# Performance work log

Hardware: AMD Instinct MI355X
Metric: run time of the kernel (lower is better)

The kernel has to match this reference:

```python
import jax, jax.numpy as jnp
import numpy as np
from jax import lax

NUM_MASK_PARAMS = 67  # 66 weights (64 feat + 2 coord channels) + 1 bias
NUM_GEN_PARAMS = 134


def _coord_maps(h, w, dtype):
    yy = jnp.broadcast_to(jnp.linspace(-1.0, 1.0, h, dtype=dtype)[:, None], (h, w))
    xx = jnp.broadcast_to(jnp.linspace(-1.0, 1.0, w, dtype=dtype)[None, :], (h, w))
    return xx, yy


def _dynamic_head(x_cat, p):
    # x_cat: [66, H, W]; p: [num_ins, 67] -> [num_ins, H, W]
    w = p[:, :NUM_MASK_PARAMS - 1]
    b = p[:, NUM_MASK_PARAMS - 1]
    return jnp.einsum('ic,chw->ihw', w, x_cat) + b[:, None, None]


def setup_inputs() -> dict:
    key = jax.random.key(0)
    ks = jax.random.split(key, 10)
    C, HM, WM, HH, WH, MB, HID = 256, 272, 480, 136, 240, 64, 64
    rn = lambda k, s, sc=1.0: jax.random.normal(k, s, dtype=jnp.float32) * sc
    return {
        'out0': rn(ks[0], (1, C, HM, WM)),
        'out1': rn(ks[1], (1, C, HH, WH)),
        'hm_w': rn(ks[2], (1, C), 0.05),
        'hm_b': jnp.zeros((1,), jnp.float32),
        'params_w': rn(ks[3], (NUM_GEN_PARAMS, C), 0.05),
        'params_b': rn(ks[4], (NUM_GEN_PARAMS,), 0.05),
        'mb_w': rn(ks[5], (MB, C, 3, 3), 0.05),
        'mb_b': jnp.zeros((MB,), jnp.float32),
        'mlp_w1': rn(ks[6], (HM, HID), 0.05),
        'mlp_b1': jnp.zeros((HID,), jnp.float32),
        'mlp_w2': rn(ks[7], (HID, 2), 0.05),
        'mlp_b2': jnp.zeros((2,), jnp.float32),
        'num_ins': 4,
    }


def reference(out0, out1, hm_w, hm_b, params_w, params_b, mb_w, mb_b,
              mlp_w1, mlp_b1, mlp_w2, mlp_b2, num_ins):
    h_mask, w_mask = out0.shape[2], out0.shape[3]
    h_hm, w_hm = out1.shape[2], out1.shape[3]

    # ctnet head: 1x1 convs on the stride-16 feature
    hm = jnp.einsum('kc,bchw->bkhw', hm_w, out1) + hm_b[None, :, None, None]
    params = jnp.einsum('kc,bchw->bkhw', params_w, out1) + params_b[None, :, None, None]
    hm = jnp.clip(jax.nn.sigmoid(hm), 1e-4, 1.0 - 1e-4)  # [1,1,h_hm,w_hm]
    # [1,134,h,w] -> [h*w, 134]
    params_flat = jnp.transpose(params[0], (1, 2, 0)).reshape(-1, NUM_GEN_PARAMS)

    # 3x3 maxpool NMS (stride 1, pad 1), keep only local peaks
    hmax = lax.reduce_window(hm, -jnp.inf, lax.max, (1, 1, 3, 3), (1, 1, 1, 1),
                             [(0, 0), (0, 0), (1, 1), (1, 1)])
    keep = (hmax == hm).astype(hm.dtype)
    heat_nms = (hm * keep).reshape(-1)

    scores, inds = lax.top_k(heat_nms, num_ins)

    # mask branch: 3x3 conv + relu on the stride-8 feature
    mask_branch = lax.conv_general_dilated(out0, mb_w, (1, 1), 'SAME',
                                           dimension_numbers=('NCHW', 'OIHW', 'NCHW'))
    mask_branch = jax.nn.relu(mask_branch + mb_b[None, :, None, None])  # [1,64,H,W]

    xx, yy = _coord_maps(h_mask, w_mask, mask_branch.dtype)
    x_cat = jnp.concatenate([mask_branch[0], xx[None], yy[None]], axis=0)  # [66,H,W]

    gen_params = params_flat[inds]  # [num_ins, 134]
    masks0 = _dynamic_head(x_cat, gen_params[:, :NUM_MASK_PARAMS])   # [num_ins,H,W]
    regs0 = _dynamic_head(x_cat, gen_params[:, NUM_MASK_PARAMS:])    # [num_ins,H,W]

    # row-wise vertical-range MLP over h_mask
    feat_range = jnp.transpose(masks0, (0, 2, 1))  # [num_ins, w_mask, h_mask]
    h1 = jax.nn.relu(feat_range @ mlp_w1 + mlp_b1)
    feat_range = h1 @ mlp_w2 + mlp_b2  # [num_ins, w_mask, 2]

    return scores, inds, regs0, masks0, feat_range
```

## Files before the change

### kernel.cpp

```cpp
#include <hip/hip_runtime.h>
#include <math.h>
#include <limits.h>

#define C_IN 256
#define HM_H 136
#define HM_W 240
#define HM_N (HM_H * HM_W)
#define MB   64
#define MH   272
#define MW   480
#define MN   (MH * MW)
#define NP   134
#define NI   4
#define HID  64

#define REG_OFF   8
#define MASK_OFF  (8 + NI * MN)
#define FEAT_OFF  (8 + 2 * NI * MN)

#define WS_HM   0
#define WS_CV   HM_N
#define WS_CI   (HM_N + 512)
#define WS_GP   (2 * HM_N)
#define WS_INDS (2 * HM_N + NI * NP)
#define WS_WT_F 65824

typedef float  f32x4  __attribute__((ext_vector_type(4)));
typedef short  bf16x8 __attribute__((ext_vector_type(8)));

__device__ __forceinline__ unsigned short f2bf(float f) {
  unsigned int u = __float_as_uint(f);
  u += 0x7FFFu + ((u >> 16) & 1u);
  return (unsigned short)(u >> 16);
}
__device__ __forceinline__ float b2f(unsigned short h) {
  return __uint_as_float(((unsigned int)h) << 16);
}

__global__ void k_wprep(const float* __restrict__ mb_w, unsigned short* __restrict__ wt) {
  int idx = blockIdx.x * 256 + threadIdx.x;
  int j    = idx & 7;
  int lane = (idx >> 3) & 63;
  int nt   = (idx >> 9) & 3;
  int gt   = idx >> 11;
  int t    = gt % 9;
  int g    = gt / 9;
  int n = nt * 16 + (lane & 15);
  int c = g * 32 + (lane >> 4) * 8 + j;
  wt[idx] = f2bf(mb_w[(n * C_IN + c) * 9 + t]);
}

__global__ void k_hm(const float* __restrict__ out1, const float* __restrict__ hm_w,
                     const float* __restrict__ hm_b, float* __restrict__ ws_hm) {
  __shared__ float part[4][64];
  int b = blockIdx.x, t = threadIdx.x;
  int cg = t >> 6, pl = t & 63;
  int p = b * 64 + pl;
  float s = 0.f;
  #pragma unroll 16
  for (int c = 0; c < 64; ++c)
    s += hm_w[cg * 64 + c] * out1[(cg * 64 + c) * HM_N + p];
  part[cg][pl] = s;
  __syncthreads();
  if (t < 64) {
    float tot = part[0][t] + part[1][t] + part[2][t] + part[3][t] + hm_b[0];
    float sig = 1.f / (1.f + expf(-tot));
    sig = fminf(fmaxf(sig, 1e-4f), 1.f - 1e-4f);
    ws_hm[b * 64 + t] = sig;
  }
}

__device__ __forceinline__ bool better(float av, int ai, float bv, int bi) {
  return (av > bv) || (av == bv && ai < bi);
}

template<int NTHR>
__device__ void top4_tree(float* sv, int* si, int t) {
  for (int s = NTHR / 2; s >= 1; s >>= 1) {
    if (t < s) {
      float a[4], b[4]; int ai[4], bj[4];
      #pragma unroll
      for (int k = 0; k < 4; ++k) {
        a[k] = sv[t * 4 + k];        ai[k] = si[t * 4 + k];
        b[k] = sv[(t + s) * 4 + k];  bj[k] = si[(t + s) * 4 + k];
      }
      float ov[4]; int oi[4];
      int i = 0, j = 0;
      #pragma unroll
      for (int k = 0; k < 4; ++k) {
        if (better(a[i], ai[i], b[j], bj[j])) { ov[k] = a[i]; oi[k] = ai[i]; ++i; }
        else                                   { ov[k] = b[j]; oi[k] = bj[j]; ++j; }
      }
      #pragma unroll
      for (int k = 0; k < 4; ++k) { sv[t * 4 + k] = ov[k]; si[t * 4 + k] = oi[k]; }
    }
    __syncthreads();
  }
}

__global__ void k_nms_top(const float* __restrict__ ws_hm, float* __restrict__ candv,
                          int* __restrict__ candi) {
  __shared__ float sv[256 * 4];
  __shared__ int   si[256 * 4];
  int b = blockIdx.x, t = threadIdx.x;
  float v = -1.f; int idx = INT_MAX;
  if (t < 255) {
    int p = b * 255 + t;
    int y = p / HM_W, x = p - y * HM_W;
    float c = ws_hm[p], m = c;
    #pragma unroll
    for (int dy = -1; dy <= 1; ++dy)
      #pragma unroll
      for (int dx = -1; dx <= 1; ++dx) {
        int yy = y + dy, xx = x + dx;
        if (yy >= 0 && yy < HM_H && xx >= 0 && xx < HM_W)
          m = fmaxf(m, ws_hm[yy * HM_W + xx]);
      }
    v = (c == m) ? c : 0.f;
    idx = p;
  }
  sv[t * 4] = v; si[t * 4] = idx;
  #pragma unroll
  for (int k = 1; k < 4; ++k) { sv[t * 4 + k] = -1.f; si[t * 4 + k] = INT_MAX; }
  __syncthreads();
  top4_tree<256>(sv, si, t);
  if (t == 0) {
    #pragma unroll
    for (int k = 0; k < 4; ++k) { candv[b * 4 + k] = sv[k]; candi[b * 4 + k] = si[k]; }
  }
}

__global__ void k_topk_final(const float* __restrict__ candv, const int* __restrict__ candi,
                             int* __restrict__ ws_inds, float* __restrict__ d_out) {
  __shared__ float sv[128 * 4];
  __shared__ int   si[128 * 4];
  int t = threadIdx.x;
  #pragma unroll
  for (int k = 0; k < 4; ++k) { sv[t * 4 + k] = candv[t * 4 + k]; si[t * 4 + k] = candi[t * 4 + k]; }
  __syncthreads();
  top4_tree<128>(sv, si, t);
  if (t == 0) {
    #pragma unroll
    for (int k = 0; k < 4; ++k) {
      d_out[k]     = sv[k];
      d_out[4 + k] = (float)si[k];
      ws_inds[k]   = si[k];
    }
  }
}

__global__ void k_gen(const float* __restrict__ out1, const float* __restrict__ params_w,
                      const float* __restrict__ params_b, const int* __restrict__ ws_inds,
                      float* __restrict__ ws_gp) {
  __shared__ float col[C_IN];
  int i = blockIdx.x;
  int p = ws_inds[i];
  col[threadIdx.x] = out1[threadIdx.x * HM_N + p];
  __syncthreads();
  int j = threadIdx.x;
  if (j < NP) {
    float s = params_b[j];
    #pragma unroll 8
    for (int c = 0; c < C_IN; ++c) s += params_w[j * C_IN + c] * col[c];
    ws_gp[i * NP + j] = s;
  }
}

#define CS 40
#define RP 36
#define BUFU 14400

__global__ __launch_bounds__(256, 2) void k_conv_mfma(
    const float* __restrict__ out0, const unsigned short* __restrict__ wt,
    const float* __restrict__ mb_b, const float* __restrict__ ws_gp,
    float* __restrict__ d_out) {
  __shared__ unsigned short smem[2 * BUFU];

  int tid  = threadIdx.x;
  int lane = tid & 63;
  int w    = tid >> 6;
  int n15  = lane & 15;
  int kq   = lane >> 4;
  int gx0 = blockIdx.x * 32, gy0 = blockIdx.y * 8;

  int goff[25], lofs[25];
  unsigned int mld = 0, mst0 = 0, mst1 = 0;
  #pragma unroll
  for (int i = 0; i < 25; ++i) {
    int u = tid + 256 * i;
    int c   = u / 200;
    int rem = u - c * 200;
    int row = rem / 20;
    int q   = rem - row * 20;
    int iy  = gy0 + row - 1;
    int ixe = gx0 + 2 * q - 2;
    bool vld = (iy >= 0) && (iy < MH) && (ixe >= 0) && (ixe < MW);
    goff[i] = vld ? (c * MN + iy * MW + ixe) : 0;
    if (vld) mld |= (1u << i);
    int x0 = 2 * q - 1;
    lofs[i] = (row * RP + x0) * CS + c;
    if (x0 >= 0 && x0 < RP)     mst0 |= (1u << i);
    if (x0 + 1 < RP)            mst1 |= (1u << i);
  }

  int rrow[4], xbas[4];
  #pragma unroll
  for (int i = 0; i < 4; ++i) {
    int mt = w * 4 + i;
    rrow[i] = mt >> 1;
    xbas[i] = (mt & 1) * 16 + n15;
  }

  {
    float2 d[25];
    #pragma unroll
    for (int i = 0; i < 25; ++i) d[i] = *(const float2*)(out0 + goff[i]);
    #pragma unroll
    for (int i = 0; i < 25; ++i) {
      bool vl = (mld >> i) & 1;
      float a = vl ? d[i].x : 0.f, bb = vl ? d[i].y : 0.f;
      if ((mst0 >> i) & 1) smem[lofs[i]]      = f2bf(a);
      if ((mst1 >> i) & 1) smem[lofs[i] + CS] = f2bf(bb);
    }
  }
  __syncthreads();

  f32x4 acc[4][4];
  #pragma unroll
  for (int i = 0; i < 4; ++i)
    #pragma unroll
    for (int nt = 0; nt < 4; ++nt)
      acc[i][nt] = (f32x4){0.f, 0.f, 0.f, 0.f};

  #pragma unroll 1
  for (int g = 0; g < 8; ++g) {
    const unsigned short* cur = smem + (g & 1) * BUFU;
    unsigned short*       nxt = smem + ((g + 1) & 1) * BUFU;
    const float*          src = out0 + (g + 1) * (32 * MN);
    float2 d[25];

    if (g < 7) {
      #pragma unroll
      for (int i = 0; i < 13; ++i) d[i] = *(const float2*)(src + goff[i]);
    }
    #pragma unroll
    for (int t = 0; t < 4; ++t) {
      int ty = t / 3, tx = t - ty * 3;
      const unsigned short* wb = wt + (g * 9 + t) * 2048 + lane * 8;
      bf16x8 bfrag[4], afrag[4];
      #pragma unroll
      for (int nt = 0; nt < 4; ++nt) bfrag[nt] = *(const bf16x8*)(wb + nt * 512);
      #pragma unroll
      for (int i = 0; i < 4; ++i)
        afrag[i] = *(const bf16x8*)&cur[((rrow[i] + ty) * RP + xbas[i] + tx) * CS + kq * 8];
      #pragma unroll
      for (int i = 0; i < 4; ++i)
        #pragma unroll
        for (int nt = 0; nt < 4; ++nt)
          acc[i][nt] = __builtin_amdgcn_mfma_f32_16x16x32_bf16(afrag[i], bfrag[nt], acc[i][nt], 0, 0, 0);
    }
    if (g < 7) {
      #pragma unroll
      for (int i = 0; i < 13; ++i) {
        bool vl = (mld >> i) & 1;
        float a = vl ? d[i].x : 0.f, bb = vl ? d[i].y : 0.f;
        if ((mst0 >> i) & 1) nxt[lofs[i]]      = f2bf(a);
        if ((mst1 >> i) & 1) nxt[lofs[i] + CS] = f2bf(bb);
      }
      #pragma unroll
      for (int i = 13; i < 25; ++i) d[i] = *(const float2*)(src + goff[i]);
    }
    #pragma unroll
    for (int t = 4; t < 9; ++t) {
      int ty = t / 3, tx = t - ty * 3;
      const unsigned short* wb = wt + (g * 9 + t) * 2048 + lane * 8;
      bf16x8 bfrag[4], afrag[4];
      #pragma unroll
      for (int nt = 0; nt < 4; ++nt) bfrag[nt] = *(const bf16x8*)(wb + nt * 512);
      #pragma unroll
      for (int i = 0; i < 4; ++i)
        afrag[i] = *(const bf16x8*)&cur[((rrow[i] + ty) * RP + xbas[i] + tx) * CS + kq * 8];
      #pragma unroll
      for (int i = 0; i < 4; ++i)
        #pragma unroll
        for (int nt = 0; nt < 4; ++nt)
          acc[i][nt] = __builtin_amdgcn_mfma_f32_16x16x32_bf16(afrag[i], bfrag[nt], acc[i][nt], 0, 0, 0);
    }
    if (g < 7) {
      #pragma unroll
      for (int i = 13; i < 25; ++i) {
        bool vl = (mld >> i) & 1;
        float a = vl ? d[i].x : 0.f, bb = vl ? d[i].y : 0.f;
        if ((mst0 >> i) & 1) nxt[lofs[i]]      = f2bf(a);
        if ((mst1 >> i) & 1) nxt[lofs[i] + CS] = f2bf(bb);
      }
    }
    __syncthreads();
  }

  #define ES 66
  float bias[4];
  #pragma unroll
  for (int nt = 0; nt < 4; ++nt) bias[nt] = mb_b[nt * 16 + n15];
  #pragma unroll
  for (int i = 0; i < 4; ++i) {
    int mt = w * 4 + i;
    int pbase = (mt >> 1) * 32 + (mt & 1) * 16;
    #pragma unroll
    for (int nt = 0; nt < 4; ++nt)
      #pragma unroll
      for (int reg = 0; reg < 4; ++reg) {
        float vv = fmaxf(acc[i][nt][reg] + bias[nt], 0.f);
        smem[(pbase + kq * 4 + reg) * ES + nt * 16 + n15] = f2bf(vv);
      }
  }
  __syncthreads();

  int r = tid >> 5, xcol = tid & 31;
  int gy = gy0 + r, gx = gx0 + xcol;
  float xc = -1.f + (2.f / 479.f) * (float)gx;
  float yc = -1.f + (2.f / 271.f) * (float)gy;
  float mres[4] = {0.f, 0.f, 0.f, 0.f};
  float rres[4] = {0.f, 0.f, 0.f, 0.f};
  #pragma unroll 8
  for (int o = 0; o < MB; ++o) {
    float v = b2f(smem[tid * ES + o]);
    #pragma unroll
    for (int i = 0; i < 4; ++i) {
      mres[i] += ws_gp[i * NP + o] * v;
      rres[i] += ws_gp[i * NP + 67 + o] * v;
    }
  }
  int pix = gy * MW + gx;
  #pragma unroll
  for (int i = 0; i < 4; ++i) {
    const float* g = ws_gp + i * NP;
    d_out[MASK_OFF + i * MN + pix] = mres[i] + g[66]  + g[64]  * xc + g[65]  * yc;
    d_out[REG_OFF  + i * MN + pix] = rres[i] + g[133] + g[131] * xc + g[132] * yc;
  }
}

__global__ void k_mlp(const float* __restrict__ masks0, const float* __restrict__ w1,
                      const float* __restrict__ b1, const float* __restrict__ w2,
                      const float* __restrict__ b2, float* __restrict__ d_out) {
  int blk = blockIdx.x;
  int i = blk / MW;
  int w = blk - i * MW;
  int k = threadIdx.x;
  const float* mcol = masks0 + i * MN + w;
  float s = b1[k];
  for (int h = 0; h < MH; ++h) s += mcol[h * MW] * w1[h * HID + k];
  s = fmaxf(s, 0.f);
  float o0 = s * w2[k * 2 + 0];
  float o1 = s * w2[k * 2 + 1];
  #pragma unroll
  for (int off = 32; off >= 1; off >>= 1) {
    o0 += __shfl_down(o0, off);
    o1 += __shfl_down(o1, off);
  }
  if (k == 0) {
    d_out[FEAT_OFF + blk * 2 + 0] = o0 + b2[0];
    d_out[FEAT_OFF + blk * 2 + 1] = o1 + b2[1];
  }
}

extern "C" void kernel_launch(void* const* d_in, const int* in_sizes, int n_in,
                              void* d_out, int out_size, void* d_ws, size_t ws_size,
                              hipStream_t stream) {
  const float* out0     = (const float*)d_in[0];
  const float* out1     = (const float*)d_in[1];
  const float* hm_w     = (const float*)d_in[2];
  const float* hm_b     = (const float*)d_in[3];
  const float* params_w = (const float*)d_in[4];
  const float* params_b = (const float*)d_in[5];
  const float* mb_w     = (const float*)d_in[6];
  const float* mb_b     = (const float*)d_in[7];
  const float* mlp_w1   = (const float*)d_in[8];
  const float* mlp_b1   = (const float*)d_in[9];
  const float* mlp_w2   = (const float*)d_in[10];
  const float* mlp_b2   = (const float*)d_in[11];

  float* ws      = (float*)d_ws;
  float* ws_hm   = ws + WS_HM;
  float* candv   = ws + WS_CV;
  int*   candi   = (int*)(ws + WS_CI);
  float* ws_gp   = ws + WS_GP;
  int*   ws_inds = (int*)(ws + WS_INDS);
  unsigned short* ws_wt = (unsigned short*)(ws + WS_WT_F);
  float* out     = (float*)d_out;

  k_wprep<<<576, 256, 0, stream>>>(mb_w, ws_wt);
  k_hm  <<<510, 256, 0, stream>>>(out1, hm_w, hm_b, ws_hm);
  k_nms_top<<<128, 256, 0, stream>>>(ws_hm, candv, candi);
  k_topk_final<<<1, 128, 0, stream>>>(candv, candi, ws_inds, out);
  k_gen <<<NI, 256, 0, stream>>>(out1, params_w, params_b, ws_inds, ws_gp);
  dim3 gconv(MW / 32, MH / 8);
  k_conv_mfma<<<gconv, 256, 0, stream>>>(out0, ws_wt, mb_b, ws_gp, out);
  k_mlp <<<NI * MW, 64, 0, stream>>>(out + MASK_OFF, mlp_w1, mlp_b1, mlp_w2, mlp_b2, out);
}
```

Baseline: 355.6 us.

## Restructure conv kernel to 512 threads with swizzled LDS and merge small kernels

The MFMA conv kernel now runs 512 threads per block (8 waves, two M-tiles each) with 16-byte vectorized global loads of four channels. Its LDS layout packs 32 channels per pixel with an XOR swizzle, and the per-pixel dynamic-head dot product is split across two thread halves, with a partial-sum reduction through shared memory. Separately, weight prep and heatmap are fused into one launch, top-k final is folded into k_gen (each block redoes the tree reduction), and the MLP loop is unrolled. The aim is to cut launch overhead, raise occupancy and MFMA overlap, and reduce LDS bank conflicts, at the cost of more blocks redundantly running top-k and new swizzle-indexing complexity.

```diff
diff --git a/kernel.cpp b/kernel.cpp
--- a/kernel.cpp
+++ b/kernel.cpp
@@ -22,11 +22,11 @@
 #define WS_CV   HM_N
 #define WS_CI   (HM_N + 512)
 #define WS_GP   (2 * HM_N)
-#define WS_INDS (2 * HM_N + NI * NP)
 #define WS_WT_F 65824
 
 typedef float  f32x4  __attribute__((ext_vector_type(4)));
 typedef short  bf16x8 __attribute__((ext_vector_type(8)));
+typedef unsigned short u16x4 __attribute__((ext_vector_type(4)));
 
 __device__ __forceinline__ unsigned short f2bf(float f) {
   unsigned int u = __float_as_uint(f);
@@ -37,36 +37,37 @@
   return __uint_as_float(((unsigned int)h) << 16);
 }
 
-__global__ void k_wprep(const float* __restrict__ mb_w, unsigned short* __restrict__ wt) {
-  int idx = blockIdx.x * 256 + threadIdx.x;
-  int j    = idx & 7;
-  int lane = (idx >> 3) & 63;
-  int nt   = (idx >> 9) & 3;
-  int gt   = idx >> 11;
-  int t    = gt % 9;
-  int g    = gt / 9;
-  int n = nt * 16 + (lane & 15);
-  int c = g * 32 + (lane >> 4) * 8 + j;
-  wt[idx] = f2bf(mb_w[(n * C_IN + c) * 9 + t]);
-}
-
-__global__ void k_hm(const float* __restrict__ out1, const float* __restrict__ hm_w,
-                     const float* __restrict__ hm_b, float* __restrict__ ws_hm) {
+__global__ void k_prep(const float* __restrict__ mb_w, unsigned short* __restrict__ wt,
+                       const float* __restrict__ out1, const float* __restrict__ hm_w,
+                       const float* __restrict__ hm_b, float* __restrict__ ws_hm) {
   __shared__ float part[4][64];
-  int b = blockIdx.x, t = threadIdx.x;
-  int cg = t >> 6, pl = t & 63;
-  int p = b * 64 + pl;
-  float s = 0.f;
-  #pragma unroll 16
-  for (int c = 0; c < 64; ++c)
-    s += hm_w[cg * 64 + c] * out1[(cg * 64 + c) * HM_N + p];
-  part[cg][pl] = s;
-  __syncthreads();
-  if (t < 64) {
-    float tot = part[0][t] + part[1][t] + part[2][t] + part[3][t] + hm_b[0];
-    float sig = 1.f / (1.f + expf(-tot));
-    sig = fminf(fmaxf(sig, 1e-4f), 1.f - 1e-4f);
-    ws_hm[b * 64 + t] = sig;
+  if (blockIdx.x < 576) {
+    int idx = blockIdx.x * 256 + threadIdx.x;
+    int j    = idx & 7;
+    int lane = (idx >> 3) & 63;
+    int nt   = (idx >> 9) & 3;
+    int gt   = idx >> 11;
+    int t    = gt % 9;
+    int g    = gt / 9;
+    int n = nt * 16 + (lane & 15);
+    int c = g * 32 + (lane >> 4) * 8 + j;
+    wt[idx] = f2bf(mb_w[(n * C_IN + c) * 9 + t]);
+  } else {
+    int b = blockIdx.x - 576, t = threadIdx.x;
+    int cg = t >> 6, pl = t & 63;
+    int p = b * 64 + pl;
+    float s = 0.f;
+    #pragma unroll 16
+    for (int c = 0; c < 64; ++c)
+      s += hm_w[cg * 64 + c] * out1[(cg * 64 + c) * HM_N + p];
+    part[cg][pl] = s;
+    __syncthreads();
+    if (t < 64) {
+      float tot = part[0][t] + part[1][t] + part[2][t] + part[3][t] + hm_b[0];
+      float sig = 1.f / (1.f + expf(-tot));
+      sig = fminf(fmaxf(sig, 1e-4f), 1.f - 1e-4f);
+      ws_hm[b * 64 + t] = sig;
+    }
   }
 }
 
@@ -130,47 +131,53 @@
   }
 }
 
-__global__ void k_topk_final(const float* __restrict__ candv, const int* __restrict__ candi,
-                             int* __restrict__ ws_inds, float* __restrict__ d_out) {
+__global__ void k_gen(const float* __restrict__ candv, const int* __restrict__ candi,
+                      const float* __restrict__ out1, const float* __restrict__ params_w,
+                      const float* __restrict__ params_b, float* __restrict__ ws_gp,
+                      float* __restrict__ d_out) {
   __shared__ float sv[128 * 4];
   __shared__ int   si[128 * 4];
-  int t = threadIdx.x;
-  #pragma unroll
-  for (int k = 0; k < 4; ++k) { sv[t * 4 + k] = candv[t * 4 + k]; si[t * 4 + k] = candi[t * 4 + k]; }
+  __shared__ float col[C_IN];
+  int t = threadIdx.x, i = blockIdx.x;
+  if (t < 128) {
+    #pragma unroll
+    for (int k = 0; k < 4; ++k) { sv[t * 4 + k] = candv[t * 4 + k]; si[t * 4 + k] = candi[t * 4 + k]; }
+  }
   __syncthreads();
   top4_tree<128>(sv, si, t);
-  if (t == 0) {
-    #pragma unroll
-    for (int k = 0; k < 4; ++k) {
-      d_out[k]     = sv[k];
-      d_out[4 + k] = (float)si[k];
-      ws_inds[k]   = si[k];
-    }
-  }
-}
-
-__global__ void k_gen(const float* __restrict__ out1, const float* __restrict__ params_w,
-                      const float* __restrict__ params_b, const int* __restrict__ ws_inds,
-                      float* __restrict__ ws_gp) {
-  __shared__ float col[C_IN];
-  int i = blockIdx.x;
-  int p = ws_inds[i];
-  col[threadIdx.x] = out1[threadIdx.x * HM_N + p];
-  __syncthreads();
-  int j = threadIdx.x;
-  if (j < NP) {
-    float s = params_b[j];
+  if (i == 0 && t < 4) {
+    d_out[t]     = sv[t];
+    d_out[4 + t] = (float)si[t];
+  }
+  int p = si[i];
+  col[t] = out1[t * HM_N + p];
+  __syncthreads();
+  if (t < NP) {
+    float s = params_b[t];
     #pragma unroll 8
-    for (int c = 0; c < C_IN; ++c) s += params_w[j * C_IN + c] * col[c];
-    ws_gp[i * NP + j] = s;
-  }
-}
-
-#define CS 40
-#define RP 36
-#define BUFU 14400
-
-__global__ __launch_bounds__(256, 2) void k_conv_mfma(
+    for (int c = 0; c < C_IN; ++c) s += params_w[t * C_IN + c] * col[c];
+    ws_gp[i * NP + t] = s;
+  }
+}
+
+#define CSU 32
+#define RP  36
+#define BUFU (10 * RP * CSU)
+
+__device__ __forceinline__ void stage_store(unsigned short* buf, const f32x4* dq,
+                                            bool gv, const int* lw, unsigned sm) {
+  #pragma unroll
+  for (int e = 0; e < 4; ++e) if ((sm >> e) & 1u) {
+    u16x4 v;
+    v[0] = f2bf(gv ? dq[0][e] : 0.f);
+    v[1] = f2bf(gv ? dq[1][e] : 0.f);
+    v[2] = f2bf(gv ? dq[2][e] : 0.f);
+    v[3] = f2bf(gv ? dq[3][e] : 0.f);
+    *(u16x4*)(buf + lw[e]) = v;
+  }
+}
+
+__global__ __launch_bounds__(512, 3) void k_conv_mfma(
     const float* __restrict__ out0, const unsigned short* __restrict__ wt,
     const float* __restrict__ mb_b, const float* __restrict__ ws_gp,
     float* __restrict__ d_out) {
@@ -178,56 +185,69 @@
 
   int tid  = threadIdx.x;
   int lane = tid & 63;
-  int w    = tid >> 6;
+  int wv   = tid >> 6;
   int n15  = lane & 15;
   int kq   = lane >> 4;
   int gx0 = blockIdx.x * 32, gy0 = blockIdx.y * 8;
 
-  int goff[25], lofs[25];
-  unsigned int mld = 0, mst0 = 0, mst1 = 0;
-  #pragma unroll
-  for (int i = 0; i < 25; ++i) {
-    int u = tid + 256 * i;
-    int c   = u / 200;
-    int rem = u - c * 200;
-    int row = rem / 20;
-    int q   = rem - row * 20;
+  int goff[2]; int lws[2][4]; unsigned smask[2]; bool gvld[2];
+  #pragma unroll
+  for (int kk = 0; kk < 2; ++kk) {
+    int u = tid + 512 * kk;
+    bool uv = (u < 800);
+    int uu = uv ? u : 0;
+    int cq  = uu / 100;
+    int rem = uu - cq * 100;
+    int row = rem / 10;
+    int qx  = rem - row * 10;
     int iy  = gy0 + row - 1;
-    int ixe = gx0 + 2 * q - 2;
-    bool vld = (iy >= 0) && (iy < MH) && (ixe >= 0) && (ixe < MW);
-    goff[i] = vld ? (c * MN + iy * MW + ixe) : 0;
-    if (vld) mld |= (1u << i);
-    int x0 = 2 * q - 1;
-    lofs[i] = (row * RP + x0) * CS + c;
-    if (x0 >= 0 && x0 < RP)     mst0 |= (1u << i);
-    if (x0 + 1 < RP)            mst1 |= (1u << i);
-  }
-
-  int rrow[4], xbas[4];
-  #pragma unroll
-  for (int i = 0; i < 4; ++i) {
-    int mt = w * 4 + i;
-    rrow[i] = mt >> 1;
-    xbas[i] = (mt & 1) * 16 + n15;
+    int ixq = gx0 + 4 * qx - 4;
+    bool v = uv && (iy >= 0) && (iy < MH) && (ixq >= 0) && (ixq + 3 < MW);
+    gvld[kk] = v;
+    goff[kk] = v ? (cq * 4 * MN + iy * MW + ixq) : 0;
+    unsigned sm = 0;
+    #pragma unroll
+    for (int e = 0; e < 4; ++e) {
+      int sx = 4 * qx - 3 + e;
+      bool s = uv && (sx >= 0) && (sx < RP);
+      int sxc = s ? sx : 0;
+      int pix = row * RP + sxc;
+      int w2  = (pix ^ (pix >> 2)) & 3;
+      lws[kk][e] = s ? ((pix << 5) + ((cq ^ (w2 << 1)) << 2)) : 0;
+      if (s) sm |= (1u << e);
+    }
+    smask[kk] = sm;
+  }
+
+  int lrd[9];
+  #pragma unroll
+  for (int t = 0; t < 9; ++t) {
+    int ty = t / 3, tx = t - ty * 3;
+    int pix = (wv + ty) * RP + n15 + tx;
+    int w2  = (pix ^ (pix >> 2)) & 3;
+    lrd[t] = (pix << 5) + ((kq ^ w2) << 3);
   }
 
   {
-    float2 d[25];
-    #pragma unroll
-    for (int i = 0; i < 25; ++i) d[i] = *(const float2*)(out0 + goff[i]);
-    #pragma unroll
-    for (int i = 0; i < 25; ++i) {
-      bool vl = (mld >> i) & 1;
-      float a = vl ? d[i].x : 0.f, bb = vl ? d[i].y : 0.f;
-      if ((mst0 >> i) & 1) smem[lofs[i]]      = f2bf(a);
-      if ((mst1 >> i) & 1) smem[lofs[i] + CS] = f2bf(bb);
-    }
-  }
-  __syncthreads();
-
-  f32x4 acc[4][4];
-  #pragma unroll
-  for (int i = 0; i < 4; ++i)
+    f32x4 dq[4];
+    {
+      const float* sp = out0 + goff[0];
+      #pragma unroll
+      for (int j = 0; j < 4; ++j) dq[j] = *(const f32x4*)(sp + j * MN);
+      stage_store(smem, dq, gvld[0], lws[0], smask[0]);
+    }
+    if (tid < 288) {
+      const float* sp = out0 + goff[1];
+      #pragma unroll
+      for (int j = 0; j < 4; ++j) dq[j] = *(const f32x4*)(sp + j * MN);
+      stage_store(smem, dq, gvld[1], lws[1], smask[1]);
+    }
+  }
+  __syncthreads();
+
+  f32x4 acc[2][4];
+  #pragma unroll
+  for (int i = 0; i < 2; ++i)
     #pragma unroll
     for (int nt = 0; nt < 4; ++nt)
       acc[i][nt] = (f32x4){0.f, 0.f, 0.f, 0.f};
@@ -237,106 +257,103 @@
     const unsigned short* cur = smem + (g & 1) * BUFU;
     unsigned short*       nxt = smem + ((g + 1) & 1) * BUFU;
     const float*          src = out0 + (g + 1) * (32 * MN);
-    float2 d[25];
+    f32x4 dqa[4], dqb[4];
 
     if (g < 7) {
-      #pragma unroll
-      for (int i = 0; i < 13; ++i) d[i] = *(const float2*)(src + goff[i]);
+      const float* sp = src + goff[0];
+      #pragma unroll
+      for (int j = 0; j < 4; ++j) dqa[j] = *(const f32x4*)(sp + j * MN);
     }
     #pragma unroll
     for (int t = 0; t < 4; ++t) {
-      int ty = t / 3, tx = t - ty * 3;
       const unsigned short* wb = wt + (g * 9 + t) * 2048 + lane * 8;
-      bf16x8 bfrag[4], afrag[4];
-      #pragma unroll
-      for (int nt = 0; nt < 4; ++nt) bfrag[nt] = *(const bf16x8*)(wb + nt * 512);
-      #pragma unroll
-      for (int i = 0; i < 4; ++i)
-        afrag[i] = *(const bf16x8*)&cur[((rrow[i] + ty) * RP + xbas[i] + tx) * CS + kq * 8];
-      #pragma unroll
-      for (int i = 0; i < 4; ++i)
+      bf16x8 bf[4];
+      #pragma unroll
+      for (int nt = 0; nt < 4; ++nt) bf[nt] = *(const bf16x8*)(wb + nt * 512);
+      bf16x8 a0 = *(const bf16x8*)&cur[lrd[t]];
+      bf16x8 a1 = *(const bf16x8*)&cur[lrd[t] + 512];
+      #pragma unroll
+      for (int nt = 0; nt < 4; ++nt) {
+        acc[0][nt] = __builtin_amdgcn_mfma_f32_16x16x32_bf16(a0, bf[nt], acc[0][nt], 0, 0, 0);
+        acc[1][nt] = __builtin_amdgcn_mfma_f32_16x16x32_bf16(a1, bf[nt], acc[1][nt], 0, 0, 0);
+      }
+    }
+    if (g < 7) {
+      stage_store(nxt, dqa, gvld[0], lws[0], smask[0]);
+      if (tid < 288) {
+        const float* sp = src + goff[1];
         #pragma unroll
-        for (int nt = 0; nt < 4; ++nt)
-          acc[i][nt] = __builtin_amdgcn_mfma_f32_16x16x32_bf16(afrag[i], bfrag[nt], acc[i][nt], 0, 0, 0);
-    }
-    if (g < 7) {
-      #pragma unroll
-      for (int i = 0; i < 13; ++i) {
-        bool vl = (mld >> i) & 1;
-        float a = vl ? d[i].x : 0.f, bb = vl ? d[i].y : 0.f;
-        if ((mst0 >> i) & 1) nxt[lofs[i]]      = f2bf(a);
-        if ((mst1 >> i) & 1) nxt[lofs[i] + CS] = f2bf(bb);
-      }
-      #pragma unroll
-      for (int i = 13; i < 25; ++i) d[i] = *(const float2*)(src + goff[i]);
+        for (int j = 0; j < 4; ++j) dqb[j] = *(const f32x4*)(sp + j * MN);
+      }
     }
     #pragma unroll
     for (int t = 4; t < 9; ++t) {
-      int ty = t / 3, tx = t - ty * 3;
       const unsigned short* wb = wt + (g * 9 + t) * 2048 + lane * 8;
-      bf16x8 bfrag[4], afrag[4];
-      #pragma unroll
-      for (int nt = 0; nt < 4; ++nt) bfrag[nt] = *(const bf16x8*)(wb + nt * 512);
-      #pragma unroll
-      for (int i = 0; i < 4; ++i)
-        afrag[i] = *(const bf16x8*)&cur[((rrow[i] + ty) * RP + xbas[i] + tx) * CS + kq * 8];
-      #pragma unroll
-      for (int i = 0; i < 4; ++i)
+      bf16x8 bf[4];
+      #pragma unroll
+      for (int nt = 0; nt < 4; ++nt) bf[nt] = *(const bf16x8*)(wb + nt * 512);
+      bf16x8 a0 = *(const bf16x8*)&cur[lrd[t]];
+      bf16x8 a1 = *(const bf16x8*)&cur[lrd[t] + 512];
+      #pragma unroll
+      for (int nt = 0; nt < 4; ++nt) {
+        acc[0][nt] = __builtin_amdgcn_mfma_f32_16x16x32_bf16(a0, bf[nt], acc[0][nt], 0, 0, 0);
+        acc[1][nt] = __builtin_amdgcn_mfma_f32_16x16x32_bf16(a1, bf[nt], acc[1][nt], 0, 0, 0);
+      }
+    }
+    if (g < 7 && tid < 288) stage_store(nxt, dqb, gvld[1], lws[1], smask[1]);
+    __syncthreads();
+  }
+
+  #define ES 66
+  {
+    float bias[4];
+    #pragma unroll
+    for (int nt = 0; nt < 4; ++nt) bias[nt] = mb_b[nt * 16 + n15];
+    #pragma unroll
+    for (int i = 0; i < 2; ++i) {
+      int pbase = wv * 32 + i * 16;
+      #pragma unroll
+      for (int nt = 0; nt < 4; ++nt)
         #pragma unroll
-        for (int nt = 0; nt < 4; ++nt)
-          acc[i][nt] = __builtin_amdgcn_mfma_f32_16x16x32_bf16(afrag[i], bfrag[nt], acc[i][nt], 0, 0, 0);
-    }
-    if (g < 7) {
-      #pragma unroll
-      for (int i = 13; i < 25; ++i) {
-        bool vl = (mld >> i) & 1;
-        float a = vl ? d[i].x : 0.f, bb = vl ? d[i].y : 0.f;
-        if ((mst0 >> i) & 1) nxt[lofs[i]]      = f2bf(a);
-        if ((mst1 >> i) & 1) nxt[lofs[i] + CS] = f2bf(bb);
-      }
-    }
-    __syncthreads();
-  }
-
-  #define ES 66
-  float bias[4];
-  #pragma unroll
-  for (int nt = 0; nt < 4; ++nt) bias[nt] = mb_b[nt * 16 + n15];
-  #pragma unroll
-  for (int i = 0; i < 4; ++i) {
-    int mt = w * 4 + i;
-    int pbase = (mt >> 1) * 32 + (mt & 1) * 16;
-    #pragma unroll
-    for (int nt = 0; nt < 4; ++nt)
-      #pragma unroll
-      for (int reg = 0; reg < 4; ++reg) {
-        float vv = fmaxf(acc[i][nt][reg] + bias[nt], 0.f);
-        smem[(pbase + kq * 4 + reg) * ES + nt * 16 + n15] = f2bf(vv);
-      }
-  }
-  __syncthreads();
-
-  int r = tid >> 5, xcol = tid & 31;
-  int gy = gy0 + r, gx = gx0 + xcol;
-  float xc = -1.f + (2.f / 479.f) * (float)gx;
-  float yc = -1.f + (2.f / 271.f) * (float)gy;
+        for (int reg = 0; reg < 4; ++reg) {
+          float vv = fmaxf(acc[i][nt][reg] + bias[nt], 0.f);
+          smem[(pbase + kq * 4 + reg) * ES + nt * 16 + n15] = f2bf(vv);
+        }
+    }
+  }
+  __syncthreads();
+
+  int p = tid & 255, hh = tid >> 8;
+  int ob = hh * 32;
   float mres[4] = {0.f, 0.f, 0.f, 0.f};
   float rres[4] = {0.f, 0.f, 0.f, 0.f};
   #pragma unroll 8
-  for (int o = 0; o < MB; ++o) {
-    float v = b2f(smem[tid * ES + o]);
+  for (int o = 0; o < 32; ++o) {
+    float v = b2f(smem[p * ES + ob + o]);
     #pragma unroll
     for (int i = 0; i < 4; ++i) {
-      mres[i] += ws_gp[i * NP + o] * v;
-      rres[i] += ws_gp[i * NP + 67 + o] * v;
-    }
-  }
-  int pix = gy * MW + gx;
-  #pragma unroll
-  for (int i = 0; i < 4; ++i) {
-    const float* g = ws_gp + i * NP;
-    d_out[MASK_OFF + i * MN + pix] = mres[i] + g[66]  + g[64]  * xc + g[65]  * yc;
-    d_out[REG_OFF  + i * MN + pix] = rres[i] + g[133] + g[131] * xc + g[132] * yc;
+      mres[i] += ws_gp[i * NP + ob + o] * v;
+      rres[i] += ws_gp[i * NP + 67 + ob + o] * v;
+    }
+  }
+  float* pf = (float*)smem + 8704;
+  if (hh) {
+    #pragma unroll
+    for (int i = 0; i < 4; ++i) { pf[p * 8 + i] = mres[i]; pf[p * 8 + 4 + i] = rres[i]; }
+  }
+  __syncthreads();
+  if (!hh) {
+    int r = p >> 5, xcol = p & 31;
+    int gy = gy0 + r, gx = gx0 + xcol;
+    float xc = -1.f + (2.f / 479.f) * (float)gx;
+    float yc = -1.f + (2.f / 271.f) * (float)gy;
+    int pix = gy * MW + gx;
+    #pragma unroll
+    for (int i = 0; i < 4; ++i) {
+      const float* gp = ws_gp + i * NP;
+      d_out[MASK_OFF + i * MN + pix] = mres[i] + pf[p * 8 + i]     + gp[66]  + gp[64]  * xc + gp[65]  * yc;
+      d_out[REG_OFF  + i * MN + pix] = rres[i] + pf[p * 8 + 4 + i] + gp[133] + gp[131] * xc + gp[132] * yc;
+    }
   }
 }
 
@@ -349,6 +366,7 @@
   int k = threadIdx.x;
   const float* mcol = masks0 + i * MN + w;
   float s = b1[k];
+  #pragma unroll 4
   for (int h = 0; h < MH; ++h) s += mcol[h * MW] * w1[h * HID + k];
   s = fmaxf(s, 0.f);
   float o0 = s * w2[k * 2 + 0];
@@ -385,16 +403,13 @@
   float* candv   = ws + WS_CV;
   int*   candi   = (int*)(ws + WS_CI);
   float* ws_gp   = ws + WS_GP;
-  int*   ws_inds = (int*)(ws + WS_INDS);
   unsigned short* ws_wt = (unsigned short*)(ws + WS_WT_F);
   float* out     = (float*)d_out;
 
-  k_wprep<<<576, 256, 0, stream>>>(mb_w, ws_wt);
-  k_hm  <<<510, 256, 0, stream>>>(out1, hm_w, hm_b, ws_hm);
+  k_prep<<<1086, 256, 0, stream>>>(mb_w, ws_wt, out1, hm_w, hm_b, ws_hm);
   k_nms_top<<<128, 256, 0, stream>>>(ws_hm, candv, candi);
-  k_topk_final<<<1, 128, 0, stream>>>(candv, candi, ws_inds, out);
-  k_gen <<<NI, 256, 0, stream>>>(out1, params_w, params_b, ws_inds, ws_gp);
+  k_gen<<<NI, 256, 0, stream>>>(candv, candi, out1, params_w, params_b, ws_gp, out);
   dim3 gconv(MW / 32, MH / 8);
-  k_conv_mfma<<<gconv, 256, 0, stream>>>(out0, ws_wt, mb_b, ws_gp, out);
-  k_mlp <<<NI * MW, 64, 0, stream>>>(out + MASK_OFF, mlp_w1, mlp_b1, mlp_w2, mlp_b2, out);
-}
+  k_conv_mfma<<<gconv, 512, 0, stream>>>(out0, ws_wt, mb_b, ws_gp, out);
+  k_mlp<<<NI * MW, 64, 0, stream>>>(out + MASK_OFF, mlp_w1, mlp_b1, mlp_w2, mlp_b2, out);
+}
```

Result: faster. 343.5 us (-3.4%).
